# Kernel tuning notes

Hardware: AMD Instinct MI355X
Metric: run time of the kernel (lower is better)

The kernel has to match this reference:

```python
import jax, jax.numpy as jnp
import numpy as np

LN_EPS = 1e-5

def _layer_norm(x, w, b):
    m = jnp.mean(x, axis=-1, keepdims=True)
    v = jnp.mean(jnp.square(x - m), axis=-1, keepdims=True)
    return (x - m) * jax.lax.rsqrt(v + LN_EPS) * w + b

def setup_inputs() -> dict:
    key = jax.random.key(0)
    ks = jax.random.split(key, 6)
    B, T, D, H = 64, 512, 512, 512
    x = jax.random.normal(ks[0], (B, T, D), dtype=jnp.float32)
    h = jax.random.normal(ks[1], (B, H), dtype=jnp.float32)
    # orthogonal-ish init approximated by scaled normal (math-equivalent shapes)
    w_ih = jax.random.normal(ks[2], (3 * H, D), dtype=jnp.float32) / np.sqrt(D)
    b_ih = jnp.zeros((3 * H,), dtype=jnp.float32)
    w_hh = jax.random.normal(ks[3], (3 * H, H), dtype=jnp.float32) / np.sqrt(H)
    b_hh = jnp.zeros((3 * H,), dtype=jnp.float32)
    ln_r_w = jnp.ones((H,), jnp.float32); ln_r_b = jnp.zeros((H,), jnp.float32)
    ln_z_w = jnp.ones((H,), jnp.float32); ln_z_b = jnp.zeros((H,), jnp.float32)
    ln_n_w = jnp.ones((H,), jnp.float32); ln_n_b = jnp.zeros((H,), jnp.float32)
    return dict(x=x, h=h, w_ih=w_ih, b_ih=b_ih, w_hh=w_hh, b_hh=b_hh,
                ln_r_w=ln_r_w, ln_r_b=ln_r_b, ln_z_w=ln_z_w, ln_z_b=ln_z_b,
                ln_n_w=ln_n_w, ln_n_b=ln_n_b)

def reference(x, h, w_ih, b_ih, w_hh, b_hh, ln_r_w, ln_r_b, ln_z_w, ln_z_b, ln_n_w, ln_n_b):
    H = h.shape[-1]
    # precompute input gate projections for all timesteps: [B, T, 3H] -> [T, B, 3H]
    x_gates_all = jnp.einsum('btd,gd->btg', x, w_ih) + b_ih
    x_gates_all = jnp.swapaxes(x_gates_all, 0, 1)

    def step(h, x_gates):
        h_gates = jnp.matmul(h, w_hh.T) + b_hh
        x_r, x_z, x_n = jnp.split(x_gates, 3, axis=-1)
        h_r, h_z, h_n = jnp.split(h_gates, 3, axis=-1)
        r = jax.nn.sigmoid(_layer_norm(x_r + h_r, ln_r_w, ln_r_b))
        z = jax.nn.sigmoid(_layer_norm(x_z + h_z, ln_z_w, ln_z_b))
        n = jnp.tanh(_layer_norm(x_n + r * h_n, ln_n_w, ln_n_b))
        h_new = (1.0 - z) * n + z * h
        return h_new, h_new

    h_last, out_tbh = jax.lax.scan(step, h, x_gates_all)
    out = jnp.swapaxes(out_tbh, 0, 1)  # [B, T, H]
    return out, h_last
```

## Files before the change

kernel.cpp:

```cpp
#include <hip/hip_runtime.h>
#include <hip/hip_bf16.h>

#define B_ 64
#define T_ 512
#define D_ 512
#define H_ 512
#define G3 1536
#define NBLK 16

typedef float f32x4 __attribute__((ext_vector_type(4)));
typedef __bf16 bf16x8 __attribute__((ext_vector_type(8)));

#define LDSP 56
#define WPITCH 520

union bfpack { bf16x8 v; __hip_bfloat16 h[8]; };

__device__ inline bf16x8 cvt8(const float* __restrict__ p) {
    float4 f0 = *(const float4*)p;
    float4 f1 = *(const float4*)(p + 4);
    bfpack u;
    u.h[0] = __float2bfloat16(f0.x); u.h[1] = __float2bfloat16(f0.y);
    u.h[2] = __float2bfloat16(f0.z); u.h[3] = __float2bfloat16(f0.w);
    u.h[4] = __float2bfloat16(f1.x); u.h[5] = __float2bfloat16(f1.y);
    u.h[6] = __float2bfloat16(f1.z); u.h[7] = __float2bfloat16(f1.w);
    return u.v;
}

__global__ void k0_init(const float* __restrict__ h_in,
                        __hip_bfloat16* __restrict__ hb,
                        unsigned int* __restrict__ ctr) {
    int i = blockIdx.x * blockDim.x + threadIdx.x;
    if (i < B_ * H_) hb[i] = __float2bfloat16(h_in[i]);
    if (i < 1024)    ctr[i] = 0u;
}

__global__ __launch_bounds__(256) void k1_xgemm(
    const float* __restrict__ X, const float* __restrict__ W,
    const float* __restrict__ bias, __hip_bfloat16* __restrict__ XG)
{
    __shared__ __align__(16) __hip_bfloat16 la[128 * LDSP];
    __shared__ __align__(16) __hip_bfloat16 lb[128 * LDSP];
    int tid = threadIdx.x, bx = blockIdx.x;
    int m0 = (bx / 12) * 128, n0 = (bx % 12) * 128;
    int wave = tid >> 6, lane = tid & 63;
    int wh = wave >> 1, ww = wave & 1;
    int l15 = lane & 15, kq = lane >> 4;

    f32x4 acc[4][4];
    #pragma unroll
    for (int i = 0; i < 4; i++)
        #pragma unroll
        for (int j = 0; j < 4; j++) acc[i][j] = (f32x4){0.f, 0.f, 0.f, 0.f};

    for (int kt = 0; kt < 16; ++kt) {
        int k0 = kt * 32;
        for (int s = tid; s < 512; s += 256) {
            int r = s >> 2, c = s & 3;
            *(bf16x8*)&la[r * LDSP + c * 8] = cvt8(&X[(size_t)(m0 + r) * D_ + k0 + c * 8]);
            *(bf16x8*)&lb[r * LDSP + c * 8] = cvt8(&W[(size_t)(n0 + r) * D_ + k0 + c * 8]);
        }
        __syncthreads();
        bf16x8 af[4], bq[4];
        #pragma unroll
        for (int i = 0; i < 4; i++)
            af[i] = *(const bf16x8*)&la[(wh * 64 + i * 16 + l15) * LDSP + kq * 8];
        #pragma unroll
        for (int j = 0; j < 4; j++)
            bq[j] = *(const bf16x8*)&lb[(ww * 64 + j * 16 + l15) * LDSP + kq * 8];
        #pragma unroll
        for (int i = 0; i < 4; i++)
            #pragma unroll
            for (int j = 0; j < 4; j++)
                acc[i][j] = __builtin_amdgcn_mfma_f32_16x16x32_bf16(af[i], bq[j], acc[i][j], 0, 0, 0);
        __syncthreads();
    }
    #pragma unroll
    for (int i = 0; i < 4; i++)
        #pragma unroll
        for (int j = 0; j < 4; j++)
            #pragma unroll
            for (int r = 0; r < 4; r++) {
                int m = m0 + wh * 64 + i * 16 + kq * 4 + r;
                int n = n0 + ww * 64 + j * 16 + l15;
                int b = m >> 9, t = m & 511;
                XG[((size_t)t * B_ + b) * G3 + n] = __float2bfloat16(acc[i][j][r] + bias[n]);
            }
}

__global__ __launch_bounds__(512, 1) void k2_recur(
    const float* __restrict__ h_in, const float* __restrict__ Whh,
    const float* __restrict__ b_hh,
    const float* __restrict__ lnrw, const float* __restrict__ lnrb,
    const float* __restrict__ lnzw, const float* __restrict__ lnzb,
    const float* __restrict__ lnnw, const float* __restrict__ lnnb,
    const __hip_bfloat16* __restrict__ XG,
    float* __restrict__ HG, __hip_bfloat16* __restrict__ HB,
    unsigned int* __restrict__ ctr, float* __restrict__ out)
{
    __shared__ __align__(16) __hip_bfloat16 lw[96 * WPITCH];
    __shared__ float sc[32];

    const int tid = threadIdx.x;
    const int blk = blockIdx.x;
    const int n0 = blk * 96;
    const int s0 = blk * 4;

    for (int idx = tid; idx < 96 * 64; idx += 512) {
        int row = idx >> 6, ch = idx & 63;
        *(bf16x8*)&lw[row * WPITCH + ch * 8] = cvt8(&Whh[(size_t)(n0 + row) * H_ + ch * 8]);
    }

    const int w = tid >> 6, lane = tid & 63;
    const int l15 = lane & 15, kq = lane >> 4;
    const int mt = w >> 1;
    const int nj0 = (w & 1) * 3;

    const int sid = tid >> 7;
    const int c = tid & 127;
    const int b = s0 + sid;

    float bhr[4], bhz[4], bhn[4], wr[4], br_[4], wz[4], bz_[4], wn[4], bn_[4], hf[4];
    #pragma unroll
    for (int j = 0; j < 4; j++) {
        int col = c + j * 128;
        bhr[j] = b_hh[col];       bhz[j] = b_hh[512 + col]; bhn[j] = b_hh[1024 + col];
        wr[j] = lnrw[col]; br_[j] = lnrb[col];
        wz[j] = lnzw[col]; bz_[j] = lnzb[col];
        wn[j] = lnnw[col]; bn_[j] = lnnb[col];
        hf[j] = h_in[b * H_ + col];
    }
    __syncthreads();

    const float inv = 1.0f / 512.0f;

    for (int t = 0; t < T_; ++t) {
        bf16x8 afr[16];
        {
            const __hip_bfloat16* hrow = HB + (mt * 16 + l15) * H_ + kq * 8;
            #pragma unroll
            for (int kt = 0; kt < 16; kt++) afr[kt] = *(const bf16x8*)(hrow + kt * 32);
        }
        f32x4 a0 = {0,0,0,0}, a1 = {0,0,0,0}, a2 = {0,0,0,0};
        #pragma unroll
        for (int kt = 0; kt < 16; kt++) {
            bf16x8 b0 = *(const bf16x8*)&lw[((nj0    ) * 16 + l15) * WPITCH + kt * 32 + kq * 8];
            bf16x8 b1 = *(const bf16x8*)&lw[((nj0 + 1) * 16 + l15) * WPITCH + kt * 32 + kq * 8];
            bf16x8 b2 = *(const bf16x8*)&lw[((nj0 + 2) * 16 + l15) * WPITCH + kt * 32 + kq * 8];
            a0 = __builtin_amdgcn_mfma_f32_16x16x32_bf16(afr[kt], b0, a0, 0, 0, 0);
            a1 = __builtin_amdgcn_mfma_f32_16x16x32_bf16(afr[kt], b1, a1, 0, 0, 0);
            a2 = __builtin_amdgcn_mfma_f32_16x16x32_bf16(afr[kt], b2, a2, 0, 0, 0);
        }
        {
            int rowb = mt * 16 + kq * 4;
            int colb = n0 + nj0 * 16 + l15;
            #pragma unroll
            for (int r = 0; r < 4; r++) {
                HG[(rowb + r) * G3 + colb     ] = a0[r];
                HG[(rowb + r) * G3 + colb + 16] = a1[r];
                HG[(rowb + r) * G3 + colb + 32] = a2[r];
            }
        }
        __syncthreads();
        if (tid == 0) {
            __threadfence();
            __hip_atomic_fetch_add(&ctr[2 * t], 1u, __ATOMIC_RELEASE, __HIP_MEMORY_SCOPE_AGENT);
            while (__hip_atomic_load(&ctr[2 * t], __ATOMIC_ACQUIRE, __HIP_MEMORY_SCOPE_AGENT) < NBLK) {}
            __threadfence();
        }
        __syncthreads();

        const float* hgrow = HG + (size_t)b * G3;
        const __hip_bfloat16* xgrow = XG + ((size_t)t * B_ + b) * G3;
        float ar[4], az[4], hgn[4], xn[4];
        float sr = 0.f, ssr = 0.f, sz = 0.f, ssz = 0.f;
        #pragma unroll
        for (int j = 0; j < 4; j++) {
            int col = c + j * 128;
            float hr = hgrow[col] + bhr[j];
            float hz = hgrow[512 + col] + bhz[j];
            hgn[j] = hgrow[1024 + col] + bhn[j];
            ar[j] = __bfloat162float(xgrow[col]) + hr;
            az[j] = __bfloat162float(xgrow[512 + col]) + hz;
            xn[j] = __bfloat162float(xgrow[1024 + col]);
            sr += ar[j]; ssr += ar[j] * ar[j];
            sz += az[j]; ssz += az[j] * az[j];
        }
        #pragma unroll
        for (int off = 32; off; off >>= 1) {
            sr += __shfl_down(sr, off); ssr += __shfl_down(ssr, off);
            sz += __shfl_down(sz, off); ssz += __shfl_down(ssz, off);
        }
        if (lane == 0) { sc[w * 4] = sr; sc[w * 4 + 1] = ssr; sc[w * 4 + 2] = sz; sc[w * 4 + 3] = ssz; }
        __syncthreads();
        {
            int w0 = sid * 2;
            sr  = sc[w0 * 4]     + sc[(w0 + 1) * 4];
            ssr = sc[w0 * 4 + 1] + sc[(w0 + 1) * 4 + 1];
            sz  = sc[w0 * 4 + 2] + sc[(w0 + 1) * 4 + 2];
            ssz = sc[w0 * 4 + 3] + sc[(w0 + 1) * 4 + 3];
        }
        __syncthreads();
        float mr = sr * inv, vr = ssr * inv - mr * mr, rstd_r = rsqrtf(vr + 1e-5f);
        float mz = sz * inv, vz = ssz * inv - mz * mz, rstd_z = rsqrtf(vz + 1e-5f);
        float rg[4], zg[4], an[4];
        float sn = 0.f, ssn = 0.f;
        #pragma unroll
        for (int j = 0; j < 4; j++) {
            rg[j] = 1.f / (1.f + __expf(-((ar[j] - mr) * rstd_r * wr[j] + br_[j])));
            zg[j] = 1.f / (1.f + __expf(-((az[j] - mz) * rstd_z * wz[j] + bz_[j])));
            an[j] = xn[j] + rg[j] * hgn[j];
            sn += an[j]; ssn += an[j] * an[j];
        }
        #pragma unroll
        for (int off = 32; off; off >>= 1) {
            sn += __shfl_down(sn, off); ssn += __shfl_down(ssn, off);
        }
        if (lane == 0) { sc[w * 4] = sn; sc[w * 4 + 1] = ssn; }
        __syncthreads();
        {
            int w0 = sid * 2;
            sn  = sc[w0 * 4]     + sc[(w0 + 1) * 4];
            ssn = sc[w0 * 4 + 1] + sc[(w0 + 1) * 4 + 1];
        }
        __syncthreads();
        float mn = sn * inv, vn = ssn * inv - mn * mn, rstd_n = rsqrtf(vn + 1e-5f);
        float hnew[4];
        #pragma unroll
        for (int j = 0; j < 4; j++) {
            float ng = tanhf((an[j] - mn) * rstd_n * wn[j] + bn_[j]);
            hnew[j] = (1.f - zg[j]) * ng + zg[j] * hf[j];
            hf[j] = hnew[j];
            HB[b * H_ + c + j * 128] = __float2bfloat16(hnew[j]);
        }
        __syncthreads();
        if (tid == 0) {
            __threadfence();
            __hip_atomic_fetch_add(&ctr[2 * t + 1], 1u, __ATOMIC_RELEASE, __HIP_MEMORY_SCOPE_AGENT);
            while (__hip_atomic_load(&ctr[2 * t + 1], __ATOMIC_ACQUIRE, __HIP_MEMORY_SCOPE_AGENT) < NBLK) {}
            __threadfence();
        }
        __syncthreads();
        #pragma unroll
        for (int j = 0; j < 4; j++)
            out[((size_t)b * T_ + t) * H_ + c + j * 128] = hnew[j];
        if (t == T_ - 1) {
            #pragma unroll
            for (int j = 0; j < 4; j++)
                out[(size_t)B_ * T_ * H_ + b * H_ + c + j * 128] = hnew[j];
        }
    }
}

extern "C" void kernel_launch(void* const* d_in, const int* in_sizes, int n_in,
                              void* d_out, int out_size, void* d_ws, size_t ws_size,
                              hipStream_t stream)
{
    const float* x    = (const float*)d_in[0];
    const float* h    = (const float*)d_in[1];
    const float* w_ih = (const float*)d_in[2];
    const float* b_ih = (const float*)d_in[3];
    const float* w_hh = (const float*)d_in[4];
    const float* b_hh = (const float*)d_in[5];
    const float* lnrw = (const float*)d_in[6];
    const float* lnrb = (const float*)d_in[7];
    const float* lnzw = (const float*)d_in[8];
    const float* lnzb = (const float*)d_in[9];
    const float* lnnw = (const float*)d_in[10];
    const float* lnnb = (const float*)d_in[11];
    float* out = (float*)d_out;

    char* ws = (char*)d_ws;
    __hip_bfloat16* XG = (__hip_bfloat16*)ws;
    float*          HG = (float*)(ws + 100663296);
    __hip_bfloat16* HB = (__hip_bfloat16*)(ws + 101056512);
    unsigned int*  CTR = (unsigned int*)(ws + 101122048);

    k0_init<<<128, 256, 0, stream>>>(h, HB, CTR);
    k1_xgemm<<<3072, 256, 0, stream>>>(x, w_ih, b_ih, XG);
    k2_recur<<<NBLK, 512, 0, stream>>>(h, w_hh, b_hh,
        lnrw, lnrb, lnzw, lnzb, lnnw, lnnb, XG, HG, HB, CTR, out);
}
```

Measured before the change: 5.607 ms.

## Use one wave per batch row for gate math and overlap loads with grid barriers

Rewrites the per-step elementwise and layernorm phase so each of the first four waves handles one batch row with 8 contiguous columns per lane. Row statistics are reduced with wave-level xor shuffles only, which removes the shared-memory partial sums and four block barriers per step. The grid barrier is split into arrive and wait: the XG loads and the output stores are issued between the atomic increment and the spin, relaxed loads plus an explicit acquire fence replace the extra thread fences, and vectorized float4 and bf16x8 accesses replace scalar ones. Half the waves sit idle during the gate phase, which trades per-step parallelism for fewer synchronizations on the serial critical path.

```diff
diff --git a/kernel.cpp b/kernel.cpp
--- a/kernel.cpp
+++ b/kernel.cpp
@@ -99,7 +99,6 @@
     unsigned int* __restrict__ ctr, float* __restrict__ out)
 {
     __shared__ __align__(16) __hip_bfloat16 lw[96 * WPITCH];
-    __shared__ float sc[32];
 
     const int tid = threadIdx.x;
     const int blk = blockIdx.x;
@@ -116,19 +115,34 @@
     const int mt = w >> 1;
     const int nj0 = (w & 1) * 3;
 
-    const int sid = tid >> 7;
-    const int c = tid & 127;
-    const int b = s0 + sid;
-
-    float bhr[4], bhz[4], bhn[4], wr[4], br_[4], wz[4], bz_[4], wn[4], bn_[4], hf[4];
-    #pragma unroll
-    for (int j = 0; j < 4; j++) {
-        int col = c + j * 128;
-        bhr[j] = b_hh[col];       bhz[j] = b_hh[512 + col]; bhn[j] = b_hh[1024 + col];
-        wr[j] = lnrw[col]; br_[j] = lnrb[col];
-        wz[j] = lnzw[col]; bz_[j] = lnzb[col];
-        wn[j] = lnnw[col]; bn_[j] = lnnb[col];
-        hf[j] = h_in[b * H_ + col];
+    const int b = s0 + w;
+    const int c0 = lane * 8;
+
+    float bhr[8], bhz[8], bhn[8], wr[8], br_[8], wz[8], bz_[8], wn[8], bn_[8], hf[8];
+    if (w < 4) {
+        #pragma unroll
+        for (int q = 0; q < 2; q++) {
+            float4 t0 = *(const float4*)&b_hh[c0 + 4 * q];
+            float4 t1 = *(const float4*)&b_hh[512 + c0 + 4 * q];
+            float4 t2 = *(const float4*)&b_hh[1024 + c0 + 4 * q];
+            float4 t3 = *(const float4*)&lnrw[c0 + 4 * q];
+            float4 t4 = *(const float4*)&lnrb[c0 + 4 * q];
+            float4 t5 = *(const float4*)&lnzw[c0 + 4 * q];
+            float4 t6 = *(const float4*)&lnzb[c0 + 4 * q];
+            float4 t7 = *(const float4*)&lnnw[c0 + 4 * q];
+            float4 t8 = *(const float4*)&lnnb[c0 + 4 * q];
+            float4 t9 = *(const float4*)&h_in[b * H_ + c0 + 4 * q];
+            bhr[4*q]=t0.x; bhr[4*q+1]=t0.y; bhr[4*q+2]=t0.z; bhr[4*q+3]=t0.w;
+            bhz[4*q]=t1.x; bhz[4*q+1]=t1.y; bhz[4*q+2]=t1.z; bhz[4*q+3]=t1.w;
+            bhn[4*q]=t2.x; bhn[4*q+1]=t2.y; bhn[4*q+2]=t2.z; bhn[4*q+3]=t2.w;
+            wr [4*q]=t3.x; wr [4*q+1]=t3.y; wr [4*q+2]=t3.z; wr [4*q+3]=t3.w;
+            br_[4*q]=t4.x; br_[4*q+1]=t4.y; br_[4*q+2]=t4.z; br_[4*q+3]=t4.w;
+            wz [4*q]=t5.x; wz [4*q+1]=t5.y; wz [4*q+2]=t5.z; wz [4*q+3]=t5.w;
+            bz_[4*q]=t6.x; bz_[4*q+1]=t6.y; bz_[4*q+2]=t6.z; bz_[4*q+3]=t6.w;
+            wn [4*q]=t7.x; wn [4*q+1]=t7.y; wn [4*q+2]=t7.z; wn [4*q+3]=t7.w;
+            bn_[4*q]=t8.x; bn_[4*q+1]=t8.y; bn_[4*q+2]=t8.z; bn_[4*q+3]=t8.w;
+            hf [4*q]=t9.x; hf [4*q+1]=t9.y; hf [4*q+2]=t9.z; hf [4*q+3]=t9.w;
+        }
     }
     __syncthreads();
 
@@ -162,93 +176,91 @@
             }
         }
         __syncthreads();
-        if (tid == 0) {
-            __threadfence();
+        if (tid == 0)
             __hip_atomic_fetch_add(&ctr[2 * t], 1u, __ATOMIC_RELEASE, __HIP_MEMORY_SCOPE_AGENT);
-            while (__hip_atomic_load(&ctr[2 * t], __ATOMIC_ACQUIRE, __HIP_MEMORY_SCOPE_AGENT) < NBLK) {}
-            __threadfence();
-        }
-        __syncthreads();
-
-        const float* hgrow = HG + (size_t)b * G3;
-        const __hip_bfloat16* xgrow = XG + ((size_t)t * B_ + b) * G3;
-        float ar[4], az[4], hgn[4], xn[4];
-        float sr = 0.f, ssr = 0.f, sz = 0.f, ssz = 0.f;
-        #pragma unroll
-        for (int j = 0; j < 4; j++) {
-            int col = c + j * 128;
-            float hr = hgrow[col] + bhr[j];
-            float hz = hgrow[512 + col] + bhz[j];
-            hgn[j] = hgrow[1024 + col] + bhn[j];
-            ar[j] = __bfloat162float(xgrow[col]) + hr;
-            az[j] = __bfloat162float(xgrow[512 + col]) + hz;
-            xn[j] = __bfloat162float(xgrow[1024 + col]);
-            sr += ar[j]; ssr += ar[j] * ar[j];
-            sz += az[j]; ssz += az[j] * az[j];
-        }
-        #pragma unroll
-        for (int off = 32; off; off >>= 1) {
-            sr += __shfl_down(sr, off); ssr += __shfl_down(ssr, off);
-            sz += __shfl_down(sz, off); ssz += __shfl_down(ssz, off);
-        }
-        if (lane == 0) { sc[w * 4] = sr; sc[w * 4 + 1] = ssr; sc[w * 4 + 2] = sz; sc[w * 4 + 3] = ssz; }
-        __syncthreads();
-        {
-            int w0 = sid * 2;
-            sr  = sc[w0 * 4]     + sc[(w0 + 1) * 4];
-            ssr = sc[w0 * 4 + 1] + sc[(w0 + 1) * 4 + 1];
-            sz  = sc[w0 * 4 + 2] + sc[(w0 + 1) * 4 + 2];
-            ssz = sc[w0 * 4 + 3] + sc[(w0 + 1) * 4 + 3];
-        }
-        __syncthreads();
-        float mr = sr * inv, vr = ssr * inv - mr * mr, rstd_r = rsqrtf(vr + 1e-5f);
-        float mz = sz * inv, vz = ssz * inv - mz * mz, rstd_z = rsqrtf(vz + 1e-5f);
-        float rg[4], zg[4], an[4];
-        float sn = 0.f, ssn = 0.f;
-        #pragma unroll
-        for (int j = 0; j < 4; j++) {
-            rg[j] = 1.f / (1.f + __expf(-((ar[j] - mr) * rstd_r * wr[j] + br_[j])));
-            zg[j] = 1.f / (1.f + __expf(-((az[j] - mz) * rstd_z * wz[j] + bz_[j])));
-            an[j] = xn[j] + rg[j] * hgn[j];
-            sn += an[j]; ssn += an[j] * an[j];
-        }
-        #pragma unroll
-        for (int off = 32; off; off >>= 1) {
-            sn += __shfl_down(sn, off); ssn += __shfl_down(ssn, off);
-        }
-        if (lane == 0) { sc[w * 4] = sn; sc[w * 4 + 1] = ssn; }
-        __syncthreads();
-        {
-            int w0 = sid * 2;
-            sn  = sc[w0 * 4]     + sc[(w0 + 1) * 4];
-            ssn = sc[w0 * 4 + 1] + sc[(w0 + 1) * 4 + 1];
-        }
-        __syncthreads();
-        float mn = sn * inv, vn = ssn * inv - mn * mn, rstd_n = rsqrtf(vn + 1e-5f);
-        float hnew[4];
-        #pragma unroll
-        for (int j = 0; j < 4; j++) {
-            float ng = tanhf((an[j] - mn) * rstd_n * wn[j] + bn_[j]);
-            hnew[j] = (1.f - zg[j]) * ng + zg[j] * hf[j];
-            hf[j] = hnew[j];
-            HB[b * H_ + c + j * 128] = __float2bfloat16(hnew[j]);
-        }
-        __syncthreads();
-        if (tid == 0) {
-            __threadfence();
+        bf16x8 xr8 = {}, xz8 = {}, xn8 = {};
+        if (w < 4) {
+            const __hip_bfloat16* xgrow = XG + ((size_t)t * B_ + b) * G3;
+            xr8 = *(const bf16x8*)&xgrow[c0];
+            xz8 = *(const bf16x8*)&xgrow[512 + c0];
+            xn8 = *(const bf16x8*)&xgrow[1024 + c0];
+        }
+        if (tid == 0)
+            while (__hip_atomic_load(&ctr[2 * t], __ATOMIC_RELAXED, __HIP_MEMORY_SCOPE_AGENT) < NBLK) {}
+        __builtin_amdgcn_fence(__ATOMIC_ACQUIRE, "agent");
+        __syncthreads();
+
+        float hnew[8];
+        if (w < 4) {
+            const float* hgb = HG + (size_t)b * G3;
+            float hr[8], hz[8], hn[8];
+            #pragma unroll
+            for (int q = 0; q < 2; q++) {
+                float4 r4 = *(const float4*)&hgb[c0 + 4 * q];
+                float4 z4 = *(const float4*)&hgb[512 + c0 + 4 * q];
+                float4 n4 = *(const float4*)&hgb[1024 + c0 + 4 * q];
+                hr[4*q]=r4.x; hr[4*q+1]=r4.y; hr[4*q+2]=r4.z; hr[4*q+3]=r4.w;
+                hz[4*q]=z4.x; hz[4*q+1]=z4.y; hz[4*q+2]=z4.z; hz[4*q+3]=z4.w;
+                hn[4*q]=n4.x; hn[4*q+1]=n4.y; hn[4*q+2]=n4.z; hn[4*q+3]=n4.w;
+            }
+            bfpack xr, xz, xn; xr.v = xr8; xz.v = xz8; xn.v = xn8;
+            float ar[8], az[8], anv[8];
+            float sr = 0.f, ssr = 0.f, sz = 0.f, ssz = 0.f;
+            #pragma unroll
+            for (int j = 0; j < 8; j++) {
+                ar[j] = __bfloat162float(xr.h[j]) + hr[j] + bhr[j];
+                az[j] = __bfloat162float(xz.h[j]) + hz[j] + bhz[j];
+                sr += ar[j]; ssr += ar[j] * ar[j];
+                sz += az[j]; ssz += az[j] * az[j];
+            }
+            #pragma unroll
+            for (int off = 32; off; off >>= 1) {
+                sr += __shfl_xor(sr, off); ssr += __shfl_xor(ssr, off);
+                sz += __shfl_xor(sz, off); ssz += __shfl_xor(ssz, off);
+            }
+            float mr = sr * inv, vr = ssr * inv - mr * mr, rstd_r = rsqrtf(vr + 1e-5f);
+            float mz = sz * inv, vz = ssz * inv - mz * mz, rstd_z = rsqrtf(vz + 1e-5f);
+            float rg[8], zg[8];
+            float sn = 0.f, ssn = 0.f;
+            #pragma unroll
+            for (int j = 0; j < 8; j++) {
+                rg[j] = 1.f / (1.f + __expf(-((ar[j] - mr) * rstd_r * wr[j] + br_[j])));
+                zg[j] = 1.f / (1.f + __expf(-((az[j] - mz) * rstd_z * wz[j] + bz_[j])));
+                anv[j] = __bfloat162float(xn.h[j]) + rg[j] * (hn[j] + bhn[j]);
+                sn += anv[j]; ssn += anv[j] * anv[j];
+            }
+            #pragma unroll
+            for (int off = 32; off; off >>= 1) {
+                sn += __shfl_xor(sn, off); ssn += __shfl_xor(ssn, off);
+            }
+            float mn = sn * inv, vn = ssn * inv - mn * mn, rstd_n = rsqrtf(vn + 1e-5f);
+            bfpack hb8;
+            #pragma unroll
+            for (int j = 0; j < 8; j++) {
+                float ng = tanhf((anv[j] - mn) * rstd_n * wn[j] + bn_[j]);
+                hnew[j] = (1.f - zg[j]) * ng + zg[j] * hf[j];
+                hf[j] = hnew[j];
+                hb8.h[j] = __float2bfloat16(hnew[j]);
+            }
+            *(bf16x8*)&HB[b * H_ + c0] = hb8.v;
+        }
+        __syncthreads();
+        if (tid == 0)
             __hip_atomic_fetch_add(&ctr[2 * t + 1], 1u, __ATOMIC_RELEASE, __HIP_MEMORY_SCOPE_AGENT);
-            while (__hip_atomic_load(&ctr[2 * t + 1], __ATOMIC_ACQUIRE, __HIP_MEMORY_SCOPE_AGENT) < NBLK) {}
-            __threadfence();
-        }
-        __syncthreads();
-        #pragma unroll
-        for (int j = 0; j < 4; j++)
-            out[((size_t)b * T_ + t) * H_ + c + j * 128] = hnew[j];
-        if (t == T_ - 1) {
-            #pragma unroll
-            for (int j = 0; j < 4; j++)
-                out[(size_t)B_ * T_ * H_ + b * H_ + c + j * 128] = hnew[j];
-        }
+        if (w < 4) {
+            float* op = out + ((size_t)b * T_ + t) * H_ + c0;
+            *(float4*)op       = make_float4(hnew[0], hnew[1], hnew[2], hnew[3]);
+            *(float4*)(op + 4) = make_float4(hnew[4], hnew[5], hnew[6], hnew[7]);
+            if (t == T_ - 1) {
+                float* fp = out + (size_t)B_ * T_ * H_ + b * H_ + c0;
+                *(float4*)fp       = make_float4(hnew[0], hnew[1], hnew[2], hnew[3]);
+                *(float4*)(fp + 4) = make_float4(hnew[4], hnew[5], hnew[6], hnew[7]);
+            }
+        }
+        if (tid == 0)
+            while (__hip_atomic_load(&ctr[2 * t + 1], __ATOMIC_RELAXED, __HIP_MEMORY_SCOPE_AGENT) < NBLK) {}
+        __builtin_amdgcn_fence(__ATOMIC_ACQUIRE, "agent");
+        __syncthreads();
     }
 }
 
```

New measurement: 5.790 ms. +3.3%, slower.
